# Optimization experiments

Measured on AMD Instinct MI355X. Metric: run time of the kernel, lower is better.

The kernel has to match this reference:

```python
import jax, jax.numpy as jnp
import numpy as np

DIM = 1024
EPS = 1e-5

def _layernorm(x, w, b):
    mu = jnp.mean(x, axis=-1, keepdims=True)
    var = jnp.var(x, axis=-1, keepdims=True)
    return (x - mu) * jax.lax.rsqrt(var + EPS) * w + b

def setup_inputs() -> dict:
    key = jax.random.key(0)
    ks = jax.random.split(key, 16)
    d = DIM
    s = 1.0 / np.sqrt(d)
    inp = {
        "x": jax.random.normal(ks[0], (4, 2048, d), dtype=jnp.float32),
        "ln1_w": jnp.ones((d,), jnp.float32),
        "ln1_b": jnp.zeros((d,), jnp.float32),
        "Wq": jax.random.normal(ks[1], (d, d), jnp.float32) * s,
        "bq": jnp.zeros((d,), jnp.float32),
        "Wk": jax.random.normal(ks[2], (d, d), jnp.float32) * s,
        "bk": jnp.zeros((d,), jnp.float32),
        "Wv": jax.random.normal(ks[3], (d, d), jnp.float32) * s,
        "bv": jnp.zeros((d,), jnp.float32),
        "Wo": jax.random.normal(ks[4], (d, d), jnp.float32) * s,
        "bo": jnp.zeros((d,), jnp.float32),
        "W1": jax.random.normal(ks[5], (d, 4 * d), jnp.float32) * s,
        "b1": jnp.zeros((4 * d,), jnp.float32),
        "W2": jax.random.normal(ks[6], (4 * d, d), jnp.float32) * (0.5 / np.sqrt(d)),
        "b2": jnp.zeros((d,), jnp.float32),
        "ln2_w": jnp.ones((d,), jnp.float32),
        "ln2_b": jnp.zeros((d,), jnp.float32),
    }
    return inp

def reference(x, ln1_w, ln1_b, Wq, bq, Wk, bk, Wv, bv, Wo, bo, W1, b1, W2, b2, ln2_w, ln2_b):
    d = x.shape[-1]
    scale = 1.0 / jnp.sqrt(jnp.asarray(d, x.dtype))
    h = _layernorm(x, ln1_w, ln1_b)
    q = h @ Wq + bq
    k = h @ Wk + bk
    v = h @ Wv + bv
    # [b, s, s] attention scores (single head, full matrix as in original)
    scores = jnp.einsum("bqd,bkd->bqk", q, k) * scale
    attn = jax.nn.softmax(scores, axis=-1)
    ctx = jnp.einsum("bqk,bkd->bqd", attn, v)
    x = x + (ctx @ Wo + bo)
    h2 = _layernorm(x, ln2_w, ln2_b)
    ffn = jax.nn.relu(h2 @ W1 + b1) @ W2 + b2
    return x + ffn
```

## Files before the change

### kernel.cpp

```cpp
#include <hip/hip_runtime.h>


#define EPS 1e-5f
constexpr int D   = 1024;
constexpr int DFF = 4096;
constexpr int NB  = 4;
constexpr int S   = 2048;
constexpr int M   = NB * S;

typedef __bf16 bf16x8 __attribute__((ext_vector_type(8)));
typedef float  f32x4  __attribute__((ext_vector_type(4)));

__device__ __forceinline__ ushort f2bf(float f) {
  uint u = __builtin_bit_cast(uint, f);
  return (ushort)((u + 0x7fffu + ((u >> 16) & 1u)) >> 16);
}
__device__ __forceinline__ float bf2f(ushort h) {
  return __builtin_bit_cast(float, (uint)h << 16);
}
__device__ __forceinline__ void split(float f, ushort& h, ushort& l) {
  h = f2bf(f);
  l = f2bf(f - bf2f(h));
}

#define GLOAD16(g, l)                                                     \
  __builtin_amdgcn_global_load_lds(                                       \
      (const __attribute__((address_space(1))) void*)(g),                 \
      (__attribute__((address_space(3))) void*)(l), 16, 0, 0)

__global__ __launch_bounds__(256) void ln_kernel(const float* __restrict__ x,
                                                 const float* __restrict__ w,
                                                 const float* __restrict__ b,
                                                 ushort* __restrict__ oh,
                                                 ushort* __restrict__ ol) {
  const int row = blockIdx.x;
  const int t   = threadIdx.x;
  const float4 v = reinterpret_cast<const float4*>(x + (size_t)row * D)[t];
  float s  = v.x + v.y + v.z + v.w;
  float sq = v.x * v.x + v.y * v.y + v.z * v.z + v.w * v.w;
#pragma unroll
  for (int off = 32; off > 0; off >>= 1) {
    s  += __shfl_down(s, off);
    sq += __shfl_down(sq, off);
  }
  __shared__ float red[8];
  if ((t & 63) == 0) { red[t >> 6] = s; red[(t >> 6) + 4] = sq; }
  __syncthreads();
  if (t == 0) {
    float ts = red[0] + red[1] + red[2] + red[3];
    float tq = red[4] + red[5] + red[6] + red[7];
    float mu  = ts * (1.0f / D);
    float var = tq * (1.0f / D) - mu * mu;
    red[0] = mu;
    red[1] = rsqrtf(var + EPS);
  }
  __syncthreads();
  const float mu = red[0], rs = red[1];
  const float4 wv = reinterpret_cast<const float4*>(w)[t];
  const float4 bv = reinterpret_cast<const float4*>(b)[t];
  float o0 = (v.x - mu) * rs * wv.x + bv.x;
  float o1 = (v.y - mu) * rs * wv.y + bv.y;
  float o2 = (v.z - mu) * rs * wv.z + bv.z;
  float o3 = (v.w - mu) * rs * wv.w + bv.w;
  ushort4 hh, ll;
  split(o0, hh.x, ll.x); split(o1, hh.y, ll.y);
  split(o2, hh.z, ll.z); split(o3, hh.w, ll.w);
  *reinterpret_cast<ushort4*>(oh + (size_t)row * D + t * 4) = hh;
  *reinterpret_cast<ushort4*>(ol + (size_t)row * D + t * 4) = ll;
}

__global__ __launch_bounds__(256) void softmax_kernel(const float* __restrict__ sc,
                                                      ushort* __restrict__ oh,
                                                      ushort* __restrict__ ol) {
  const size_t row = blockIdx.x;
  const float* p = sc + row * (size_t)S;
  const int t = threadIdx.x;
  constexpr float scale = 0.03125f;
  float4 a = reinterpret_cast<const float4*>(p)[t];
  float4 b = reinterpret_cast<const float4*>(p)[t + 256];
  a.x *= scale; a.y *= scale; a.z *= scale; a.w *= scale;
  b.x *= scale; b.y *= scale; b.z *= scale; b.w *= scale;
  float m = fmaxf(fmaxf(fmaxf(a.x, a.y), fmaxf(a.z, a.w)),
                  fmaxf(fmaxf(b.x, b.y), fmaxf(b.z, b.w)));
#pragma unroll
  for (int off = 32; off > 0; off >>= 1) m = fmaxf(m, __shfl_xor(m, off));
  __shared__ float redm[4];
  __shared__ float reds[4];
  if ((t & 63) == 0) redm[t >> 6] = m;
  __syncthreads();
  m = fmaxf(fmaxf(redm[0], redm[1]), fmaxf(redm[2], redm[3]));
  a.x = __expf(a.x - m); a.y = __expf(a.y - m);
  a.z = __expf(a.z - m); a.w = __expf(a.w - m);
  b.x = __expf(b.x - m); b.y = __expf(b.y - m);
  b.z = __expf(b.z - m); b.w = __expf(b.w - m);
  float s = a.x + a.y + a.z + a.w + b.x + b.y + b.z + b.w;
#pragma unroll
  for (int off = 32; off > 0; off >>= 1) s += __shfl_xor(s, off);
  if ((t & 63) == 0) reds[t >> 6] = s;
  __syncthreads();
  s = reds[0] + reds[1] + reds[2] + reds[3];
  const float inv = 1.0f / s;
  ushort4 ha, la, hb, lb;
  split(a.x * inv, ha.x, la.x); split(a.y * inv, ha.y, la.y);
  split(a.z * inv, ha.z, la.z); split(a.w * inv, ha.w, la.w);
  split(b.x * inv, hb.x, lb.x); split(b.y * inv, hb.y, lb.y);
  split(b.z * inv, hb.z, lb.z); split(b.w * inv, hb.w, lb.w);
  ushort* ph = oh + row * (size_t)S;
  ushort* pl = ol + row * (size_t)S;
  *reinterpret_cast<ushort4*>(ph + t * 4)        = ha;
  *reinterpret_cast<ushort4*>(ph + 1024 + t * 4) = hb;
  *reinterpret_cast<ushort4*>(pl + t * 4)        = la;
  *reinterpret_cast<ushort4*>(pl + 1024 + t * 4) = lb;
}

__global__ __launch_bounds__(256) void transpose_conv(const float* __restrict__ in,
                                                      ushort* __restrict__ oh,
                                                      ushort* __restrict__ ol,
                                                      int R, int C,
                                                      long long sIn, long long sOut) {
  __shared__ float tile[32][33];
  const int bz = blockIdx.z;
  const float* ip = in + (size_t)bz * sIn;
  ushort* ph = oh + (size_t)bz * sOut;
  ushort* pl = ol + (size_t)bz * sOut;
  const int c0 = blockIdx.x * 32, r0 = blockIdx.y * 32;
  const int tx = threadIdx.x & 31, ty = threadIdx.x >> 5;
#pragma unroll
  for (int i = 0; i < 4; ++i)
    tile[ty + 8 * i][tx] = ip[(size_t)(r0 + ty + 8 * i) * C + c0 + tx];
  __syncthreads();
#pragma unroll
  for (int i = 0; i < 4; ++i) {
    float v = tile[tx][ty + 8 * i];
    ushort h, l;
    split(v, h, l);
    const size_t o = (size_t)(c0 + ty + 8 * i) * R + r0 + tx;
    ph[o] = h;
    pl[o] = l;
  }
}

template <bool HAS_BIAS, bool RELU, bool HAS_RES, bool WRITE_F32, bool EMIT_BF16>
__global__ __launch_bounds__(256, 2) void gemm_bf16x3(
    const ushort* __restrict__ Ah, const ushort* __restrict__ Al,
    const ushort* __restrict__ Bth, const ushort* __restrict__ Btl,
    const float* __restrict__ bias, const float* Res,
    float* Cf, ushort* __restrict__ Ch, ushort* __restrict__ Cl,
    int N, int K, long long sA, long long sB, long long sC) {
  __shared__ __align__(16) ushort sAh[128 * 32];
  __shared__ __align__(16) ushort sAl[128 * 32];
  __shared__ __align__(16) ushort sBh[128 * 32];
  __shared__ __align__(16) ushort sBl[128 * 32];

  const int bz = blockIdx.z;
  const size_t aof = (size_t)bz * sA, bof = (size_t)bz * sB, cof = (size_t)bz * sC;

  const int gx = gridDim.x;
  const int nwg = gx * gridDim.y;
  int lin = blockIdx.y * gx + blockIdx.x;
  lin = (lin & 7) * (nwg >> 3) + (lin >> 3);
  const int bm = (lin / gx) * 128;
  const int bn = (lin % gx) * 128;

  const int tid = threadIdx.x, w = tid >> 6, lane = tid & 63;
  const int wr = (w >> 1) * 64, wc = (w & 1) * 64;

  const int c0 = w * 2, c1 = c0 + 1;
  const int r0 = c0 * 16 + (lane >> 2);
  const int r1 = r0 + 16;
  const int kc = ((lane & 3) ^ (r0 & 3)) * 8;
  const size_t gA0 = aof + (size_t)(bm + r0) * K + kc;
  const size_t gA1 = aof + (size_t)(bm + r1) * K + kc;
  const size_t gB0 = bof + (size_t)(bn + r0) * K + kc;
  const size_t gB1 = bof + (size_t)(bn + r1) * K + kc;
  ushort* dA0 = sAh + c0 * 512; ushort* dA1 = sAh + c1 * 512;
  ushort* dA2 = sAl + c0 * 512; ushort* dA3 = sAl + c1 * 512;
  ushort* dB0 = sBh + c0 * 512; ushort* dB1 = sBh + c1 * 512;
  ushort* dB2 = sBl + c0 * 512; ushort* dB3 = sBl + c1 * 512;

  const int fr = lane & 15, fc = lane >> 4;
  int aoffB[4], boffB[4];
#pragma unroll
  for (int i = 0; i < 4; ++i) {
    const int ra = wr + i * 16 + fr;
    aoffB[i] = ra * 64 + ((fc ^ (ra & 3)) * 16);
    const int rb = wc + i * 16 + fr;
    boffB[i] = rb * 64 + ((fc ^ (rb & 3)) * 16);
  }

  f32x4 acc[4][4];
  const f32x4 zero = {0.f, 0.f, 0.f, 0.f};
#pragma unroll
  for (int i = 0; i < 4; ++i)
#pragma unroll
    for (int j = 0; j < 4; ++j) acc[i][j] = zero;

  for (int kk = 0; kk < K; kk += 32) {
    GLOAD16(Ah + gA0 + kk, dA0);
    GLOAD16(Ah + gA1 + kk, dA1);
    GLOAD16(Al + gA0 + kk, dA2);
    GLOAD16(Al + gA1 + kk, dA3);
    GLOAD16(Bth + gB0 + kk, dB0);
    GLOAD16(Bth + gB1 + kk, dB1);
    GLOAD16(Btl + gB0 + kk, dB2);
    GLOAD16(Btl + gB1 + kk, dB3);
    __syncthreads();

    bf16x8 fah[4], fal[4], fbh[4], fbl[4];
#pragma unroll
    for (int i = 0; i < 4; ++i) {
      fah[i] = __builtin_bit_cast(bf16x8,
          *reinterpret_cast<const uint4*>(reinterpret_cast<const char*>(sAh) + aoffB[i]));
      fal[i] = __builtin_bit_cast(bf16x8,
          *reinterpret_cast<const uint4*>(reinterpret_cast<const char*>(sAl) + aoffB[i]));
      fbh[i] = __builtin_bit_cast(bf16x8,
          *reinterpret_cast<const uint4*>(reinterpret_cast<const char*>(sBh) + boffB[i]));
      fbl[i] = __builtin_bit_cast(bf16x8,
          *reinterpret_cast<const uint4*>(reinterpret_cast<const char*>(sBl) + boffB[i]));
    }
    __syncthreads();

#pragma unroll
    for (int i = 0; i < 4; ++i)
#pragma unroll
      for (int j = 0; j < 4; ++j) {
        acc[i][j] = __builtin_amdgcn_mfma_f32_16x16x32_bf16(fah[i], fbh[j], acc[i][j], 0, 0, 0);
        acc[i][j] = __builtin_amdgcn_mfma_f32_16x16x32_bf16(fah[i], fbl[j], acc[i][j], 0, 0, 0);
        acc[i][j] = __builtin_amdgcn_mfma_f32_16x16x32_bf16(fal[i], fbh[j], acc[i][j], 0, 0, 0);
      }
  }

#pragma unroll
  for (int j = 0; j < 4; ++j) {
    const int col = bn + wc + j * 16 + fr;
    const float bi = HAS_BIAS ? bias[col] : 0.0f;
#pragma unroll
    for (int i = 0; i < 4; ++i) {
#pragma unroll
      for (int r = 0; r < 4; ++r) {
        const int row = bm + wr + i * 16 + fc * 4 + r;
        float o = acc[i][j][r] + bi;
        if (RELU) o = fmaxf(o, 0.0f);
        const size_t idx = cof + (size_t)row * N + col;
        if (HAS_RES) o += Res[idx];
        if (WRITE_F32) Cf[idx] = o;
        if (EMIT_BF16) {
          ushort h, l;
          split(o, h, l);
          Ch[idx] = h;
          Cl[idx] = l;
        }
      }
    }
  }
}

extern "C" void kernel_launch(void* const* d_in, const int* in_sizes, int n_in,
                              void* d_out, int out_size, void* d_ws, size_t ws_size,
                              hipStream_t stream) {
  const float* x     = (const float*)d_in[0];
  const float* ln1_w = (const float*)d_in[1];
  const float* ln1_b = (const float*)d_in[2];
  const float* Wq    = (const float*)d_in[3];
  const float* bq    = (const float*)d_in[4];
  const float* Wk    = (const float*)d_in[5];
  const float* bk    = (const float*)d_in[6];
  const float* Wv    = (const float*)d_in[7];
  const float* bv    = (const float*)d_in[8];
  const float* Wo    = (const float*)d_in[9];
  const float* bo    = (const float*)d_in[10];
  const float* W1    = (const float*)d_in[11];
  const float* b1    = (const float*)d_in[12];
  const float* W2    = (const float*)d_in[13];
  const float* b2    = (const float*)d_in[14];
  const float* ln2_w = (const float*)d_in[15];
  const float* ln2_b = (const float*)d_in[16];
  float* out = (float*)d_out;
  char* W = (char*)d_ws;

  auto U = [&](size_t mb) { return (ushort*)(W + (mb << 20)); };
  auto F = [&](size_t mb) { return (float*)(W + (mb << 20)); };
  ushort *h1h = U(0),   *h1l = U(16);
  ushort *wqh = U(32),  *wql = U(34);
  ushort *wkh = U(36),  *wkl = U(38);
  ushort *wvh = U(40),  *wvl = U(42);
  ushort *qh  = U(64),  *ql  = U(80);
  ushort *kh  = U(96),  *kl  = U(112);
  float  *vf  = F(128);
  ushort *vth = U(160), *vtl = U(176);
  float  *scf = F(0);
  ushort *ath = U(64),  *atl = U(96);
  ushort *cxh = U(128), *cxl = U(144);
  ushort *woh = U(0),   *wol = U(2);
  ushort *h2h = U(32),  *h2l = U(48);
  ushort *w1h = U(0),   *w1l = U(8);
  ushort *w2h = U(16),  *w2l = U(24);
  ushort *t1h = U(64),  *t1l = U(128);

  const long long SD = (long long)S * D, SS = (long long)S * S;
  dim3 tb(256);

  transpose_conv<<<dim3(32, 32, 1), tb, 0, stream>>>(Wq, wqh, wql, D, D, 0, 0);
  transpose_conv<<<dim3(32, 32, 1), tb, 0, stream>>>(Wk, wkh, wkl, D, D, 0, 0);
  transpose_conv<<<dim3(32, 32, 1), tb, 0, stream>>>(Wv, wvh, wvl, D, D, 0, 0);

  ln_kernel<<<M, tb, 0, stream>>>(x, ln1_w, ln1_b, h1h, h1l);

  dim3 g1024(D / 128, M / 128, 1);
  gemm_bf16x3<true, false, false, false, true><<<g1024, tb, 0, stream>>>(
      h1h, h1l, wqh, wql, bq, nullptr, nullptr, qh, ql, D, D, 0, 0, 0);
  gemm_bf16x3<true, false, false, false, true><<<g1024, tb, 0, stream>>>(
      h1h, h1l, wkh, wkl, bk, nullptr, nullptr, kh, kl, D, D, 0, 0, 0);
  gemm_bf16x3<true, false, false, true, false><<<g1024, tb, 0, stream>>>(
      h1h, h1l, wvh, wvl, bv, nullptr, vf, nullptr, nullptr, D, D, 0, 0, 0);

  transpose_conv<<<dim3(D / 32, S / 32, NB), tb, 0, stream>>>(vf, vth, vtl, S, D, SD, SD);

  dim3 gsc(S / 128, S / 128, NB);
  gemm_bf16x3<false, false, false, true, false><<<gsc, tb, 0, stream>>>(
      qh, ql, kh, kl, nullptr, nullptr, scf, nullptr, nullptr, S, D, SD, SD, SS);

  softmax_kernel<<<M, tb, 0, stream>>>(scf, ath, atl);

  dim3 gcx(D / 128, S / 128, NB);
  gemm_bf16x3<false, false, false, false, true><<<gcx, tb, 0, stream>>>(
      ath, atl, vth, vtl, nullptr, nullptr, nullptr, cxh, cxl, D, S, SS, SD, SD);

  transpose_conv<<<dim3(32, 32, 1), tb, 0, stream>>>(Wo, woh, wol, D, D, 0, 0);
  gemm_bf16x3<true, false, true, true, false><<<g1024, tb, 0, stream>>>(
      cxh, cxl, woh, wol, bo, x, out, nullptr, nullptr, D, D, 0, 0, 0);

  ln_kernel<<<M, tb, 0, stream>>>(out, ln2_w, ln2_b, h2h, h2l);

  transpose_conv<<<dim3(DFF / 32, D / 32, 1), tb, 0, stream>>>(W1, w1h, w1l, D, DFF, 0, 0);
  transpose_conv<<<dim3(D / 32, DFF / 32, 1), tb, 0, stream>>>(W2, w2h, w2l, DFF, D, 0, 0);

  dim3 gf1(DFF / 128, M / 128, 1);
  gemm_bf16x3<true, true, false, false, true><<<gf1, tb, 0, stream>>>(
      h2h, h2l, w1h, w1l, b1, nullptr, nullptr, t1h, t1l, DFF, D, 0, 0, 0);

  gemm_bf16x3<true, false, true, true, false><<<g1024, tb, 0, stream>>>(
      t1h, t1l, w2h, w2l, b2, out, out, nullptr, nullptr, D, DFF, 0, 0, 0);
}
```

Measured before the change: 1.068 ms.

## Add double-buffered 256x256 bf16x3 GEMM, fuse QKV projections and emit bf16 V

Adds a new 512-thread GEMM kernel with 256x256 tiles, a double-buffered LDS pipeline with interleaved global prefetch, an XOR-swizzled shared layout and raised priority around the MFMA bursts. It is used for a single fused QKV projection that writes three segments, for the QK^T scores and for the FFN up-projection. The V projection now emits split bf16 directly and is transposed by a new bf16 transpose, which removes the fp32 V round trip. Workspace buffers are reshuffled to make room. Larger tiles cut global traffic per FLOP but raise register and LDS pressure and reduce the number of workgroups for the smaller GEMMs.

```diff
diff --git a/kernel.cpp b/kernel.cpp
--- a/kernel.cpp
+++ b/kernel.cpp
@@ -27,6 +27,9 @@
   __builtin_amdgcn_global_load_lds(                                       \
       (const __attribute__((address_space(1))) void*)(g),                 \
       (__attribute__((address_space(3))) void*)(l), 16, 0, 0)
+
+#define LD8(base, off) \
+  __builtin_bit_cast(bf16x8, *reinterpret_cast<const uint4*>((base) + (off)))
 
 __global__ __launch_bounds__(256) void ln_kernel(const float* __restrict__ x,
                                                  const float* __restrict__ w,
@@ -140,6 +143,230 @@
   }
 }
 
+__global__ __launch_bounds__(256) void transpose_bf(const ushort* __restrict__ ih,
+                                                    const ushort* __restrict__ il,
+                                                    ushort* __restrict__ oh,
+                                                    ushort* __restrict__ ol,
+                                                    int R, int C,
+                                                    long long sIn, long long sOut) {
+  __shared__ ushort th[32][34];
+  __shared__ ushort tl[32][34];
+  const int bz = blockIdx.z;
+  const ushort* ph = ih + (size_t)bz * sIn;
+  const ushort* pl = il + (size_t)bz * sIn;
+  ushort* qh = oh + (size_t)bz * sOut;
+  ushort* ql = ol + (size_t)bz * sOut;
+  const int c0 = blockIdx.x * 32, r0 = blockIdx.y * 32;
+  const int tx = threadIdx.x & 31, ty = threadIdx.x >> 5;
+#pragma unroll
+  for (int i = 0; i < 4; ++i) {
+    const size_t src = (size_t)(r0 + ty + 8 * i) * C + c0 + tx;
+    th[ty + 8 * i][tx] = ph[src];
+    tl[ty + 8 * i][tx] = pl[src];
+  }
+  __syncthreads();
+#pragma unroll
+  for (int i = 0; i < 4; ++i) {
+    const size_t o = (size_t)(c0 + ty + 8 * i) * R + r0 + tx;
+    qh[o] = th[tx][ty + 8 * i];
+    ql[o] = tl[tx][ty + 8 * i];
+  }
+}
+
+template <bool HAS_BIAS, bool RELU, bool WRITE_F32, int NSEG>
+__global__ __launch_bounds__(512, 2) void gemm256(
+    const ushort* __restrict__ Ah, const ushort* __restrict__ Al,
+    const ushort* __restrict__ Bth, const ushort* __restrict__ Btl,
+    const float* __restrict__ b0, const float* __restrict__ b1,
+    const float* __restrict__ b2, float* __restrict__ Cf,
+    ushort* __restrict__ Ch0, ushort* __restrict__ Cl0,
+    ushort* __restrict__ Ch1, ushort* __restrict__ Cl1,
+    ushort* __restrict__ Ch2, ushort* __restrict__ Cl2,
+    int N, int K, int ostride, long long sA, long long sB, long long sC) {
+  __shared__ __align__(16) ushort sAb[2][256 * 64];
+  __shared__ __align__(16) ushort sBb[2][256 * 64];
+
+  const int bz = blockIdx.z;
+  const size_t aof = (size_t)bz * sA, bof = (size_t)bz * sB, cof = (size_t)bz * sC;
+
+  const int gx = gridDim.x;
+  const int nwg = gx * gridDim.y;
+  int lin = blockIdx.y * gx + blockIdx.x;
+  lin = (lin & 7) * (nwg >> 3) + (lin >> 3);
+  const int bm = (lin / gx) * 256;
+  const int bn = (lin % gx) * 256;
+
+  const int tid = threadIdx.x;
+  const int lane = tid & 63, w = tid >> 6;
+  const int wr = (w >> 2) * 128, wc = (w & 3) * 64;
+  const int fr = lane & 15, fc = lane >> 4;
+
+  const int srow  = tid >> 3;
+  const int slot  = (tid & 7) ^ (srow & 7);
+  const int hilo  = slot >> 2;
+  const int kg    = slot & 3;
+  const ushort* gA = (hilo ? Al : Ah) + aof + (size_t)(bm + srow) * K + kg * 8;
+  const ushort* gB = (hilo ? Btl : Bth) + bof + (size_t)(bn + srow) * K + kg * 8;
+  const size_t rstep = (size_t)64 * K;
+  const int dsto = tid * 16;
+
+  int aoff[8][2], boff[4][2];
+#pragma unroll
+  for (int i = 0; i < 8; ++i) {
+    const int row = wr + i * 16 + fr;
+#pragma unroll
+    for (int h = 0; h < 2; ++h)
+      aoff[i][h] = row * 128 + (((h * 4 + fc) ^ (row & 7)) * 16);
+  }
+#pragma unroll
+  for (int j = 0; j < 4; ++j) {
+    const int row = wc + j * 16 + fr;
+#pragma unroll
+    for (int h = 0; h < 2; ++h)
+      boff[j][h] = row * 128 + (((h * 4 + fc) ^ (row & 7)) * 16);
+  }
+
+  f32x4 acc[8][4];
+  const f32x4 zero = {0.f, 0.f, 0.f, 0.f};
+#pragma unroll
+  for (int i = 0; i < 8; ++i)
+#pragma unroll
+    for (int j = 0; j < 4; ++j) acc[i][j] = zero;
+
+  const int nt = K >> 5;
+
+  {
+    char* dA = (char*)(&sAb[0][0]) + dsto;
+    char* dB = (char*)(&sBb[0][0]) + dsto;
+#pragma unroll
+    for (int rr = 0; rr < 4; ++rr) {
+      GLOAD16(gA + rr * rstep, dA + rr * 8192);
+      GLOAD16(gB + rr * rstep, dB + rr * 8192);
+    }
+  }
+
+#define MFMA6(ii, xh, xl, jj)                                                 \
+  acc[ii][jj] = __builtin_amdgcn_mfma_f32_16x16x32_bf16(xh, bh##jj, acc[ii][jj], 0, 0, 0); \
+  acc[ii][jj] = __builtin_amdgcn_mfma_f32_16x16x32_bf16(xh, bl##jj, acc[ii][jj], 0, 0, 0); \
+  acc[ii][jj] = __builtin_amdgcn_mfma_f32_16x16x32_bf16(xl, bh##jj, acc[ii][jj], 0, 0, 0);
+
+#define MFMA_PAIR(i0, i1, xh, xl, yh, yl)                                     \
+  MFMA6(i0, xh, xl, 0) MFMA6(i1, yh, yl, 0)                                   \
+  MFMA6(i0, xh, xl, 1) MFMA6(i1, yh, yl, 1)                                   \
+  MFMA6(i0, xh, xl, 2) MFMA6(i1, yh, yl, 2)                                   \
+  MFMA6(i0, xh, xl, 3) MFMA6(i1, yh, yl, 3)
+
+  for (int t = 0; t < nt; ++t) {
+    const int p = t & 1, q = p ^ 1;
+    const bool pf = (t + 1 < nt);
+    const int kkn = (t + 1) << 5;
+    const ushort* gAn = gA + kkn;
+    const ushort* gBn = gB + kkn;
+    char* dAq = (char*)(&sAb[q][0]) + dsto;
+    char* dBq = (char*)(&sBb[q][0]) + dsto;
+    const char* lA = (const char*)(&sAb[p][0]);
+    const char* lB = (const char*)(&sBb[p][0]);
+
+    if (pf) {
+      GLOAD16(gAn + 0 * rstep, dAq + 0 * 8192);
+      GLOAD16(gAn + 1 * rstep, dAq + 1 * 8192);
+      asm volatile("s_waitcnt vmcnt(2)" ::: "memory");
+    } else {
+      asm volatile("s_waitcnt vmcnt(0)" ::: "memory");
+    }
+    __builtin_amdgcn_s_barrier();
+
+    bf16x8 bh0 = LD8(lB, boff[0][0]), bl0 = LD8(lB, boff[0][1]);
+    bf16x8 bh1 = LD8(lB, boff[1][0]), bl1 = LD8(lB, boff[1][1]);
+    bf16x8 bh2 = LD8(lB, boff[2][0]), bl2 = LD8(lB, boff[2][1]);
+    bf16x8 bh3 = LD8(lB, boff[3][0]), bl3 = LD8(lB, boff[3][1]);
+    bf16x8 a0h = LD8(lA, aoff[0][0]), a0l = LD8(lA, aoff[0][1]);
+    bf16x8 a1h = LD8(lA, aoff[1][0]), a1l = LD8(lA, aoff[1][1]);
+    __builtin_amdgcn_s_barrier();
+    __builtin_amdgcn_s_setprio(1);
+    MFMA_PAIR(0, 1, a0h, a0l, a1h, a1l)
+    __builtin_amdgcn_s_setprio(0);
+    __builtin_amdgcn_s_barrier();
+
+    {
+      bf16x8 a2h = LD8(lA, aoff[2][0]), a2l = LD8(lA, aoff[2][1]);
+      bf16x8 a3h = LD8(lA, aoff[3][0]), a3l = LD8(lA, aoff[3][1]);
+      if (pf) {
+        GLOAD16(gAn + 2 * rstep, dAq + 2 * 8192);
+        GLOAD16(gAn + 3 * rstep, dAq + 3 * 8192);
+      }
+      __builtin_amdgcn_s_barrier();
+      __builtin_amdgcn_s_setprio(1);
+      MFMA_PAIR(2, 3, a2h, a2l, a3h, a3l)
+      __builtin_amdgcn_s_setprio(0);
+      __builtin_amdgcn_s_barrier();
+    }
+    {
+      bf16x8 a4h = LD8(lA, aoff[4][0]), a4l = LD8(lA, aoff[4][1]);
+      bf16x8 a5h = LD8(lA, aoff[5][0]), a5l = LD8(lA, aoff[5][1]);
+      if (pf) {
+        GLOAD16(gBn + 0 * rstep, dBq + 0 * 8192);
+        GLOAD16(gBn + 1 * rstep, dBq + 1 * 8192);
+      }
+      __builtin_amdgcn_s_barrier();
+      __builtin_amdgcn_s_setprio(1);
+      MFMA_PAIR(4, 5, a4h, a4l, a5h, a5l)
+      __builtin_amdgcn_s_setprio(0);
+      __builtin_amdgcn_s_barrier();
+    }
+    {
+      bf16x8 a6h = LD8(lA, aoff[6][0]), a6l = LD8(lA, aoff[6][1]);
+      bf16x8 a7h = LD8(lA, aoff[7][0]), a7l = LD8(lA, aoff[7][1]);
+      if (pf) {
+        GLOAD16(gBn + 2 * rstep, dBq + 2 * 8192);
+        GLOAD16(gBn + 3 * rstep, dBq + 3 * 8192);
+      }
+      __builtin_amdgcn_s_barrier();
+      __builtin_amdgcn_s_setprio(1);
+      MFMA_PAIR(6, 7, a6h, a6l, a7h, a7l)
+      __builtin_amdgcn_s_setprio(0);
+      __builtin_amdgcn_s_barrier();
+    }
+  }
+
+#pragma unroll
+  for (int j = 0; j < 4; ++j) {
+    const int col = bn + wc + j * 16 + fr;
+    int lc = col;
+    const float* bp = b0;
+    ushort* ph = Ch0;
+    ushort* pl = Cl0;
+    if (NSEG == 3) {
+      const int seg = col >> 10;
+      lc = col & 1023;
+      bp = (seg == 0) ? b0 : (seg == 1 ? b1 : b2);
+      ph = (seg == 0) ? Ch0 : (seg == 1 ? Ch1 : Ch2);
+      pl = (seg == 0) ? Cl0 : (seg == 1 ? Cl1 : Cl2);
+    }
+    const float bi = HAS_BIAS ? bp[lc] : 0.0f;
+#pragma unroll
+    for (int i = 0; i < 8; ++i) {
+#pragma unroll
+      for (int r = 0; r < 4; ++r) {
+        const int row = bm + wr + i * 16 + fc * 4 + r;
+        float o = acc[i][j][r] + bi;
+        if (RELU) o = fmaxf(o, 0.0f);
+        if (WRITE_F32) {
+          Cf[cof + (size_t)row * N + col] = o;
+        } else {
+          ushort hh, ll;
+          split(o, hh, ll);
+          const size_t idx = (size_t)row * ostride + lc;
+          ph[idx] = hh;
+          pl[idx] = ll;
+        }
+      }
+    }
+  }
+#undef MFMA6
+#undef MFMA_PAIR
+}
+
 template <bool HAS_BIAS, bool RELU, bool HAS_RES, bool WRITE_F32, bool EMIT_BF16>
 __global__ __launch_bounds__(256, 2) void gemm_bf16x3(
     const ushort* __restrict__ Ah, const ushort* __restrict__ Al,
@@ -209,14 +436,10 @@
     bf16x8 fah[4], fal[4], fbh[4], fbl[4];
 #pragma unroll
     for (int i = 0; i < 4; ++i) {
-      fah[i] = __builtin_bit_cast(bf16x8,
-          *reinterpret_cast<const uint4*>(reinterpret_cast<const char*>(sAh) + aoffB[i]));
-      fal[i] = __builtin_bit_cast(bf16x8,
-          *reinterpret_cast<const uint4*>(reinterpret_cast<const char*>(sAl) + aoffB[i]));
-      fbh[i] = __builtin_bit_cast(bf16x8,
-          *reinterpret_cast<const uint4*>(reinterpret_cast<const char*>(sBh) + boffB[i]));
-      fbl[i] = __builtin_bit_cast(bf16x8,
-          *reinterpret_cast<const uint4*>(reinterpret_cast<const char*>(sBl) + boffB[i]));
+      fah[i] = LD8((const char*)sAh, aoffB[i]);
+      fal[i] = LD8((const char*)sAl, aoffB[i]);
+      fbh[i] = LD8((const char*)sBh, boffB[i]);
+      fbl[i] = LD8((const char*)sBl, boffB[i]);
     }
     __syncthreads();
 
@@ -281,64 +504,61 @@
   auto U = [&](size_t mb) { return (ushort*)(W + (mb << 20)); };
   auto F = [&](size_t mb) { return (float*)(W + (mb << 20)); };
   ushort *h1h = U(0),   *h1l = U(16);
-  ushort *wqh = U(32),  *wql = U(34);
-  ushort *wkh = U(36),  *wkl = U(38);
-  ushort *wvh = U(40),  *wvl = U(42);
+  ushort *wqkvh = U(32), *wqkvl = U(38);
   ushort *qh  = U(64),  *ql  = U(80);
   ushort *kh  = U(96),  *kl  = U(112);
-  float  *vf  = F(128);
+  ushort *vh  = U(128), *vl  = U(144);
   ushort *vth = U(160), *vtl = U(176);
   float  *scf = F(0);
   ushort *ath = U(64),  *atl = U(96);
   ushort *cxh = U(128), *cxl = U(144);
   ushort *woh = U(0),   *wol = U(2);
-  ushort *h2h = U(32),  *h2l = U(48);
-  ushort *w1h = U(0),   *w1l = U(8);
-  ushort *w2h = U(16),  *w2l = U(24);
+  ushort *h2h = U(4),   *h2l = U(20);
+  ushort *w1h = U(36),  *w1l = U(44);
+  ushort *w2h = U(0),   *w2l = U(8);
   ushort *t1h = U(64),  *t1l = U(128);
 
   const long long SD = (long long)S * D, SS = (long long)S * S;
   dim3 tb(256);
 
-  transpose_conv<<<dim3(32, 32, 1), tb, 0, stream>>>(Wq, wqh, wql, D, D, 0, 0);
-  transpose_conv<<<dim3(32, 32, 1), tb, 0, stream>>>(Wk, wkh, wkl, D, D, 0, 0);
-  transpose_conv<<<dim3(32, 32, 1), tb, 0, stream>>>(Wv, wvh, wvl, D, D, 0, 0);
+  transpose_conv<<<dim3(32, 32, 1), tb, 0, stream>>>(Wq, wqkvh, wqkvl, D, D, 0, 0);
+  transpose_conv<<<dim3(32, 32, 1), tb, 0, stream>>>(Wk, wqkvh + (size_t)D * D,
+                                                     wqkvl + (size_t)D * D, D, D, 0, 0);
+  transpose_conv<<<dim3(32, 32, 1), tb, 0, stream>>>(Wv, wqkvh + 2 * (size_t)D * D,
+                                                     wqkvl + 2 * (size_t)D * D, D, D, 0, 0);
 
   ln_kernel<<<M, tb, 0, stream>>>(x, ln1_w, ln1_b, h1h, h1l);
 
-  dim3 g1024(D / 128, M / 128, 1);
-  gemm_bf16x3<true, false, false, false, true><<<g1024, tb, 0, stream>>>(
-      h1h, h1l, wqh, wql, bq, nullptr, nullptr, qh, ql, D, D, 0, 0, 0);
-  gemm_bf16x3<true, false, false, false, true><<<g1024, tb, 0, stream>>>(
-      h1h, h1l, wkh, wkl, bk, nullptr, nullptr, kh, kl, D, D, 0, 0, 0);
-  gemm_bf16x3<true, false, false, true, false><<<g1024, tb, 0, stream>>>(
-      h1h, h1l, wvh, wvl, bv, nullptr, vf, nullptr, nullptr, D, D, 0, 0, 0);
-
-  transpose_conv<<<dim3(D / 32, S / 32, NB), tb, 0, stream>>>(vf, vth, vtl, S, D, SD, SD);
-
-  dim3 gsc(S / 128, S / 128, NB);
-  gemm_bf16x3<false, false, false, true, false><<<gsc, tb, 0, stream>>>(
-      qh, ql, kh, kl, nullptr, nullptr, scf, nullptr, nullptr, S, D, SD, SD, SS);
+  gemm256<true, false, false, 3><<<dim3(12, 32, 1), 512, 0, stream>>>(
+      h1h, h1l, wqkvh, wqkvl, bq, bk, bv, nullptr,
+      qh, ql, kh, kl, vh, vl, 3072, D, D, 0, 0, 0);
+
+  transpose_bf<<<dim3(32, 64, NB), tb, 0, stream>>>(vh, vl, vth, vtl, S, D, SD, SD);
+
+  gemm256<false, false, true, 1><<<dim3(8, 8, NB), 512, 0, stream>>>(
+      qh, ql, kh, kl, nullptr, nullptr, nullptr, scf,
+      nullptr, nullptr, nullptr, nullptr, nullptr, nullptr,
+      S, D, S, SD, SD, SS);
 
   softmax_kernel<<<M, tb, 0, stream>>>(scf, ath, atl);
 
-  dim3 gcx(D / 128, S / 128, NB);
-  gemm_bf16x3<false, false, false, false, true><<<gcx, tb, 0, stream>>>(
+  gemm_bf16x3<false, false, false, false, true><<<dim3(8, 16, NB), tb, 0, stream>>>(
       ath, atl, vth, vtl, nullptr, nullptr, nullptr, cxh, cxl, D, S, SS, SD, SD);
 
   transpose_conv<<<dim3(32, 32, 1), tb, 0, stream>>>(Wo, woh, wol, D, D, 0, 0);
-  gemm_bf16x3<true, false, true, true, false><<<g1024, tb, 0, stream>>>(
+  gemm_bf16x3<true, false, true, true, false><<<dim3(8, 64, 1), tb, 0, stream>>>(
       cxh, cxl, woh, wol, bo, x, out, nullptr, nullptr, D, D, 0, 0, 0);
 
   ln_kernel<<<M, tb, 0, stream>>>(out, ln2_w, ln2_b, h2h, h2l);
 
-  transpose_conv<<<dim3(DFF / 32, D / 32, 1), tb, 0, stream>>>(W1, w1h, w1l, D, DFF, 0, 0);
-  transpose_conv<<<dim3(D / 32, DFF / 32, 1), tb, 0, stream>>>(W2, w2h, w2l, DFF, D, 0, 0);
-
-  dim3 gf1(DFF / 128, M / 128, 1);
-  gemm_bf16x3<true, true, false, false, true><<<gf1, tb, 0, stream>>>(
-      h2h, h2l, w1h, w1l, b1, nullptr, nullptr, t1h, t1l, DFF, D, 0, 0, 0);
-
-  gemm_bf16x3<true, false, true, true, false><<<g1024, tb, 0, stream>>>(
+  transpose_conv<<<dim3(128, 32, 1), tb, 0, stream>>>(W1, w1h, w1l, D, DFF, 0, 0);
+
+  gemm256<true, true, false, 1><<<dim3(16, 32, 1), 512, 0, stream>>>(
+      h2h, h2l, w1h, w1l, b1, nullptr, nullptr, nullptr,
+      t1h, t1l, nullptr, nullptr, nullptr, nullptr, DFF, D, DFF, 0, 0, 0);
+
+  transpose_conv<<<dim3(32, 128, 1), tb, 0, stream>>>(W2, w2h, w2l, DFF, D, 0, 0);
+
+  gemm_bf16x3<true, false, true, true, false><<<dim3(8, 64, 1), tb, 0, stream>>>(
       t1h, t1l, w2h, w2l, b2, out, out, nullptr, nullptr, D, DFF, 0, 0, 0);
 }
```

New measurement: 1.075 ms. About the same (+0.6%).
